# Kernel optimization log

Measured on AMD Instinct MI355X. Metric: run time of the kernel, lower is better.

The kernel has to match this reference:

```python
import jax, jax.numpy as jnp
import numpy as np

B, N, C_IN, C_OUT, K, KS = 8, 2048, 64, 64, 20, 20


def _paiconv(x, feature, kernals, one_padding, mlp_w, mlp_b, conv_w, conv_b,
             mlp_out_w, mlp_out_b, bn_gamma, bn_beta):
    b, c, n = feature.shape
    pts = jnp.transpose(x, (0, 2, 1))                       # [B,N,3]
    sq = jnp.sum(pts * pts, axis=-1)                        # [B,N]
    d2 = sq[:, :, None] + sq[:, None, :] - 2.0 * jnp.einsum('bnd,bmd->bnm', pts, pts)
    _, idx = jax.lax.top_k(-d2, K)                          # [B,N,K] nearest (self first)
    bidx = jnp.arange(b)[:, None, None]
    x_neighs = pts[bidx, idx].reshape(b * n, K, 3)          # [BN,K,3]
    x_repeat = jnp.broadcast_to(x_neighs[:, :1, :], x_neighs.shape)
    x_rel = x_neighs - x_repeat                             # [BN,K,3]
    x_dis = jnp.sqrt(jnp.sum(x_rel * x_rel, axis=-1, keepdims=True) + 1e-12)
    x_feats7 = jnp.concatenate([x_repeat, x_rel, x_dis], axis=-1)  # [BN,K,7]
    # pointwise MLP (Conv1d 7->in_c, kernel 1)
    x_feats = jnp.einsum('nkc,oc->nok', x_feats7, mlp_w) + mlp_b[None, :, None]  # [BN,C,K]
    featsT = jnp.transpose(feature, (0, 2, 1))              # [B,N,C]
    neigh_feats = featsT[bidx, idx].reshape(b * n, K, c)    # [BN,K,C]
    feats = jnp.concatenate([jnp.transpose(neigh_feats, (0, 2, 1)), x_feats], axis=1)  # [BN,2C,K]
    # permutation matrix with threshold + double normalization (topkmax)
    perm = jnp.einsum('nkd,dm->nkm', x_rel, kernals) + one_padding  # [BN,K,KS]
    perm = jnp.where(perm > 0, perm, 0.0)
    perm = perm / (jnp.sum(perm, axis=1, keepdims=True) + 1e-6)
    perm = perm * perm
    perm = perm / (jnp.sum(perm, axis=1, keepdims=True) + 1e-6)
    perm = jnp.where(perm > 0.1, perm, 0.0)
    agg = jnp.einsum('nck,nkm->ncm', feats, perm).reshape(b * n, 2 * c * KS)
    out = (agg @ conv_w.T + conv_b).reshape(b, n, C_OUT)
    out = jnp.transpose(out, (0, 2, 1)) \
        + jnp.einsum('bcn,oc->bon', feature, mlp_out_w) + mlp_out_b[None, :, None]
    # BatchNorm1d (training-mode batch stats, biased variance, eps=1e-5)
    mean = jnp.mean(out, axis=(0, 2), keepdims=True)
    var = jnp.var(out, axis=(0, 2), keepdims=True)
    out = (out - mean) / jnp.sqrt(var + 1e-5)
    return out * bn_gamma[None, :, None] + bn_beta[None, :, None]


def setup_inputs() -> dict:
    key = jax.random.key(0)
    ks = jax.random.split(key, 10)
    one_padding = jnp.zeros((K, KS), jnp.float32).at[0, 0].set(1.0)
    return {
        'x': jax.random.normal(ks[0], (B, 3, N), jnp.float32),
        'feature': jax.random.normal(ks[1], (B, C_IN, N), jnp.float32),
        'kernals': jax.random.normal(ks[2], (3, KS), jnp.float32),
        'one_padding': one_padding,
        'mlp_w': jax.random.normal(ks[3], (C_IN, 7), jnp.float32) * 0.2,
        'mlp_b': jnp.zeros((C_IN,), jnp.float32),
        'conv_w': jax.random.normal(ks[4], (C_OUT, 2 * C_IN * KS), jnp.float32) * 0.02,
        'conv_b': jnp.zeros((C_OUT,), jnp.float32),
        'mlp_out_w': jax.random.normal(ks[5], (C_OUT, C_IN), jnp.float32) * 0.1,
        'mlp_out_b': jnp.zeros((C_OUT,), jnp.float32),
        'bn_gamma': jnp.ones((C_OUT,), jnp.float32),
        'bn_beta': jnp.zeros((C_OUT,), jnp.float32),
    }


def reference(x, feature, kernals, one_padding, mlp_w, mlp_b, conv_w, conv_b,
              mlp_out_w, mlp_out_b, bn_gamma, bn_beta):
    return _paiconv(x, feature, kernals, one_padding, mlp_w, mlp_b, conv_w, conv_b,
                    mlp_out_w, mlp_out_b, bn_gamma, bn_beta)
```

## Files before the change

kernel.cpp:

```cpp
#include <hip/hip_runtime.h>
#include <cstddef>

#define BB   8
#define NN   2048
#define CIN  64
#define COUT 64
#define KK   20
#define KSS  20
#define C2   128
#define PPB  4
#define NC   24
#define KT   80
#define AGG_LD 2576

typedef _Float16 h2t  __attribute__((ext_vector_type(2)));
typedef _Float16 f16x8 __attribute__((ext_vector_type(8)));
typedef float    f32x4 __attribute__((ext_vector_type(4)));

__device__ __forceinline__ unsigned pk2(float a, float b) {
    unsigned short ua = __builtin_bit_cast(unsigned short, (_Float16)a);
    unsigned short ub = __builtin_bit_cast(unsigned short, (_Float16)b);
    return (unsigned)ua | ((unsigned)ub << 16);
}

__device__ __forceinline__ unsigned wave_min_u32(unsigned v) {
    unsigned x = v, t;
    t = (unsigned)__builtin_amdgcn_update_dpp((int)x, (int)x, 0x111, 0xf, 0xf, false);
    x = (t < x) ? t : x;
    t = (unsigned)__builtin_amdgcn_update_dpp((int)x, (int)x, 0x112, 0xf, 0xf, false);
    x = (t < x) ? t : x;
    t = (unsigned)__builtin_amdgcn_update_dpp((int)x, (int)x, 0x114, 0xf, 0xf, false);
    x = (t < x) ? t : x;
    t = (unsigned)__builtin_amdgcn_update_dpp((int)x, (int)x, 0x118, 0xf, 0xf, false);
    x = (t < x) ? t : x;
    t = (unsigned)__builtin_amdgcn_update_dpp((int)x, (int)x, 0x142, 0xf, 0xf, false);
    x = (t < x) ? t : x;
    t = (unsigned)__builtin_amdgcn_update_dpp((int)x, (int)x, 0x143, 0xf, 0xf, false);
    x = (t < x) ? t : x;
    return (unsigned)__builtin_amdgcn_readlane((int)x, 63);
}

__global__ __launch_bounds__(256) void prep_kernel(
    const float* __restrict__ cw, const float* __restrict__ mw,
    uint4* __restrict__ aFrag, float* __restrict__ mowT)
{
    int i = blockIdx.x * 256 + threadIdx.x;
    if (i < 4 * KT * 64) {
        int wv = i / (KT * 64);
        int r  = i - wv * (KT * 64);
        int t  = r >> 6, l = r & 63;
        int o  = (wv << 4) + (l & 15);
        int j  = (t << 5) + ((l >> 4) << 3);
        const float* s = cw + (size_t)o * (C2 * KSS) + j;
        uint4 v;
        v.x = pk2(s[0], s[1]);
        v.y = pk2(s[2], s[3]);
        v.z = pk2(s[4], s[5]);
        v.w = pk2(s[6], s[7]);
        aFrag[i] = v;
    }
    if (i < COUT * CIN) {
        int o = i >> 6, c = i & 63;
        mowT[c * COUT + o] = mw[o * CIN + c];
    }
}

__global__ __launch_bounds__(256) void tr_kernel(
    const float* __restrict__ f, float* __restrict__ ft)
{
    __shared__ float tile[64][65];
    const int bt = blockIdx.x;
    const int b  = bt >> 5;
    const int n0 = (bt & 31) << 6;
    const int tn  = threadIdx.x & 63;
    const int tc0 = threadIdx.x >> 6;
#pragma unroll
    for (int r = 0; r < 16; ++r) {
        int c = (r << 2) + tc0;
        tile[c][tn] = f[((size_t)(b * CIN + c)) * NN + n0 + tn];
    }
    __syncthreads();
#pragma unroll
    for (int r = 0; r < 16; ++r) {
        int n = (r << 2) + tc0;
        ft[((size_t)b * NN + n0 + n) * CIN + tn] = tile[tn][n];
    }
}

__global__ __launch_bounds__(256, 4) void knn_kernel(
    const float* __restrict__ x, int* __restrict__ nid)
{
    const int tid  = threadIdx.x;
    const int w    = tid >> 6;
    const int lane = tid & 63;
    const int p    = blockIdx.x * 4 + w;
    const int b    = p >> 11;
    const int n    = p & (NN - 1);

    const float* xb0 = x + (size_t)(b * 3 + 0) * NN;
    const float* xb1 = x + (size_t)(b * 3 + 1) * NN;
    const float* xb2 = x + (size_t)(b * 3 + 2) * NN;

    const unsigned long long SENT = 0xFFFFFFFFFFFFFFFFull;
    const float qx = xb0[n], qy = xb1[n], qz = xb2[n];

    float d2r[32];
#pragma unroll
    for (int j = 0; j < 32; ++j) {
        int m = lane + 64 * j;
        float dx = xb0[m] - qx;
        float dy = xb1[m] - qy;
        float dz = xb2[m] - qz;
        d2r[j] = dx * dx + dy * dy + dz * dz;
    }

    unsigned long long c0 = SENT, c1 = SENT, c2 = SENT;
#pragma unroll
    for (int j = 0; j < 32; ++j) {
        unsigned long long pk =
            ((unsigned long long)__float_as_uint(d2r[j]) << 32)
            | (unsigned)(lane + 64 * j);
        if (pk < c0)      { c2 = c1; c1 = c0; c0 = pk; }
        else if (pk < c1) { c2 = c1; c1 = pk; }
        else if (pk < c2) { c2 = pk; }
    }

    unsigned killmask = 0u;
    unsigned long long mypk = SENT;
    for (int k = 0; k < NC; ++k) {
        unsigned myd  = (unsigned)(c0 >> 32);
        unsigned dmin = wave_min_u32(myd);
        unsigned idxc = (myd == dmin) ? (unsigned)c0 : 0xFFFFFFFFu;
        unsigned imin = wave_min_u32(idxc);
        unsigned long long bp = ((unsigned long long)dmin << 32) | imin;

        if (lane == k) mypk = bp;
        if (c0 == bp) {
            killmask |= 1u << ((unsigned)(bp & 0xFFFFFFFFull) >> 6);
            c0 = c1; c1 = c2; c2 = SENT;
            if (c0 == SENT) {
#pragma unroll
                for (int j = 0; j < 32; ++j) {
                    if (!(killmask & (1u << j))) {
                        unsigned long long pk =
                            ((unsigned long long)__float_as_uint(d2r[j]) << 32)
                            | (unsigned)(lane + 64 * j);
                        if (pk < c0)      { c2 = c1; c1 = c0; c0 = pk; }
                        else if (pk < c1) { c2 = c1; c1 = pk; }
                        else if (pk < c2) { c2 = pk; }
                    }
                }
            }
        }
    }

    double dd = 1e300;
    int ci = 0x7fffffff;
    if (lane < NC) {
        ci = (int)(mypk & 0xFFFFFFFFull);
        double dx = (double)xb0[ci] - (double)qx;
        double dy = (double)xb1[ci] - (double)qy;
        double dz = (double)xb2[ci] - (double)qz;
        dd = dx * dx + dy * dy + dz * dz;
    }
    unsigned long long db = __double_as_longlong(dd);
#pragma unroll
    for (int size = 2; size <= 32; size <<= 1) {
#pragma unroll
        for (int stride = size >> 1; stride > 0; stride >>= 1) {
            unsigned long long odb = __shfl_xor(db, stride);
            int oci = __shfl_xor(ci, stride);
            bool up = ((lane & size) == 0);
            bool takemin = (((lane & stride) == 0) == up);
            bool oless = (odb < db) || (odb == db && oci < ci);
            if (takemin == oless) { db = odb; ci = oci; }
        }
    }
    if (lane < KK) nid[(size_t)p * KK + lane] = ci;
}

__global__ __launch_bounds__(256, 3) void point_kernel(
    const float* __restrict__ x,
    const float* __restrict__ featT,
    const float* __restrict__ kern,
    const float* __restrict__ pad,
    const float* __restrict__ mlp_w,
    const float* __restrict__ mlp_b,
    const uint4* __restrict__ aFrag,
    const float* __restrict__ conv_b,
    const float* __restrict__ mowT,
    const float* __restrict__ mob,
    const int* __restrict__ nid,
    float* __restrict__ out)
{
    __shared__ __align__(16) _Float16 agg_h[PPB][AGG_LD];
    __shared__ __align__(16) float u_s[PPB * KK * KSS];
    __shared__ float xr_s[PPB][KK][3];
    __shared__ float xd_s[PPB][KK];
    __shared__ float xrep_s[PPB][3];
    __shared__ float colden_s[PPB][KSS];
    __shared__ float fcol_s[PPB][CIN];
    __shared__ int   nid_s[PPB][KK];

    float (*perm_s)[KK][KSS] = (float (*)[KK][KSS])u_s;
    float (*red2)[COUT]      = (float (*)[COUT])u_s;

    const int tid  = threadIdx.x;
    const int w    = tid >> 6;
    const int lane = tid & 63;
    const int p    = blockIdx.x * PPB + w;
    const int b    = p >> 11;
    const int n    = p & (NN - 1);

    const float* xb0 = x + (size_t)(b * 3 + 0) * NN;
    const float* xb1 = x + (size_t)(b * 3 + 1) * NN;
    const float* xb2 = x + (size_t)(b * 3 + 2) * NN;

    if (lane < KK) nid_s[w][lane] = nid[(size_t)p * KK + lane];

    fcol_s[w][lane] = featT[((size_t)b * NN + n) * CIN + lane];

    if (lane == 0) {
        int m0 = nid_s[w][0];
        xrep_s[w][0] = xb0[m0]; xrep_s[w][1] = xb1[m0]; xrep_s[w][2] = xb2[m0];
    }
    if (lane < KK) {
        int m = nid_s[w][lane];
        float rx = xb0[m] - xrep_s[w][0];
        float ry = xb1[m] - xrep_s[w][1];
        float rz = xb2[m] - xrep_s[w][2];
        xr_s[w][lane][0] = rx; xr_s[w][lane][1] = ry; xr_s[w][lane][2] = rz;
        xd_s[w][lane] = sqrtf(rx * rx + ry * ry + rz * rz + 1e-12f);
    }

    for (int e = lane; e < KK * KSS; e += 64) {
        int k = e / KSS, m = e % KSS;
        float v = xr_s[w][k][0] * kern[0 * KSS + m]
                + xr_s[w][k][1] * kern[1 * KSS + m]
                + xr_s[w][k][2] * kern[2 * KSS + m]
                + pad[k * KSS + m];
        perm_s[w][k][m] = v > 0.0f ? v : 0.0f;
    }
    if (lane < KSS) {
        float s = 0.0f;
        for (int k = 0; k < KK; ++k) s += perm_s[w][k][lane];
        colden_s[w][lane] = s + 1e-6f;
    }
    for (int e = lane; e < KK * KSS; e += 64) {
        int k = e / KSS, m = e % KSS;
        float v = perm_s[w][k][m] / colden_s[w][m];
        perm_s[w][k][m] = v * v;
    }
    if (lane < KSS) {
        float s = 0.0f;
        for (int k = 0; k < KK; ++k) s += perm_s[w][k][lane];
        colden_s[w][lane] = s + 1e-6f;
    }
    for (int e = lane; e < KK * KSS; e += 64) {
        int k = e / KSS, m = e % KSS;
        float v = perm_s[w][k][m] / colden_s[w][m];
        perm_s[w][k][m] = v > 0.1f ? v : 0.0f;
    }

    float fg[KK], fm[KK];
#pragma unroll
    for (int k = 0; k < KK; ++k)
        fg[k] = featT[((size_t)b * NN + nid_s[w][k]) * CIN + lane];
    {
        float w0 = mlp_w[lane * 7 + 0], w1 = mlp_w[lane * 7 + 1];
        float w2 = mlp_w[lane * 7 + 2], w3 = mlp_w[lane * 7 + 3];
        float w4 = mlp_w[lane * 7 + 4], w5 = mlp_w[lane * 7 + 5];
        float w6 = mlp_w[lane * 7 + 6];
        float bias = mlp_b[lane];
#pragma unroll
        for (int k = 0; k < KK; ++k) {
            fm[k] = xrep_s[w][0] * w0 + xrep_s[w][1] * w1 + xrep_s[w][2] * w2
                  + xr_s[w][k][0] * w3 + xr_s[w][k][1] * w4 + xr_s[w][k][2] * w5
                  + xd_s[w][k] * w6 + bias;
        }
    }

#pragma unroll
    for (int m4 = 0; m4 < KSS / 4; ++m4) {
        float sx = 0.f, sy = 0.f, sz = 0.f, sw = 0.f;
        float tx = 0.f, ty = 0.f, tz = 0.f, tw = 0.f;
#pragma unroll
        for (int k = 0; k < KK; ++k) {
            const float4 pv = *(const float4*)&perm_s[w][k][m4 * 4];
            const float a = fg[k], c = fm[k];
            sx += a * pv.x; sy += a * pv.y; sz += a * pv.z; sw += a * pv.w;
            tx += c * pv.x; ty += c * pv.y; tz += c * pv.z; tw += c * pv.w;
        }
        const int mb = m4 * 4;
        agg_h[w][lane * KSS + mb + 0]         = (_Float16)sx;
        agg_h[w][lane * KSS + mb + 1]         = (_Float16)sy;
        agg_h[w][lane * KSS + mb + 2]         = (_Float16)sz;
        agg_h[w][lane * KSS + mb + 3]         = (_Float16)sw;
        agg_h[w][(CIN + lane) * KSS + mb + 0] = (_Float16)tx;
        agg_h[w][(CIN + lane) * KSS + mb + 1] = (_Float16)ty;
        agg_h[w][(CIN + lane) * KSS + mb + 2] = (_Float16)tz;
        agg_h[w][(CIN + lane) * KSS + mb + 3] = (_Float16)tw;
    }
    __syncthreads();

    {
        f32x4 acc0 = {0.f, 0.f, 0.f, 0.f};
        f32x4 acc1 = {0.f, 0.f, 0.f, 0.f};
        const uint4* ap = aFrag + (size_t)(w * KT) * 64 + lane;
        const _Float16* bp = &agg_h[lane & 3][(lane >> 4) * 8];
#pragma unroll 4
        for (int t = 0; t < KT; t += 2) {
            uint4 av0 = ap[(size_t)t * 64];
            uint4 av1 = ap[(size_t)(t + 1) * 64];
            f16x8 b0 = *(const f16x8*)(bp + t * 32);
            f16x8 b1 = *(const f16x8*)(bp + (t + 1) * 32);
            acc0 = __builtin_amdgcn_mfma_f32_16x16x32_f16(
                       __builtin_bit_cast(f16x8, av0), b0, acc0, 0, 0, 0);
            acc1 = __builtin_amdgcn_mfma_f32_16x16x32_f16(
                       __builtin_bit_cast(f16x8, av1), b1, acc1, 0, 0, 0);
        }
        acc0 += acc1;
        if ((lane & 15) < 4) {
            const int p2 = lane & 15;
            const int ob = (w << 4) + ((lane >> 4) << 2);
            *(f32x4*)&red2[p2][ob] = acc0;
        }
    }
    __syncthreads();

    {
        float acc = conv_b[lane] + red2[w][lane];
        for (int c = 0; c < CIN; ++c)
            acc += fcol_s[w][c] * mowT[c * COUT + lane];
        acc += mob[lane];
        out[(size_t)(b * COUT + lane) * NN + n] = acc;
    }
}

__global__ __launch_bounds__(256) void bn_reduce(
    const float* __restrict__ out, float* __restrict__ part)
{
    const int o = blockIdx.x >> 3;
    const int s = blockIdx.x & 7;
    const float* src = out + (size_t)(s * COUT + o) * NN;
    float a = 0.f, q = 0.f;
    for (int i = threadIdx.x; i < NN; i += 256) {
        float v = src[i];
        a += v; q += v * v;
    }
    __shared__ float s1[256], s2[256];
    s1[threadIdx.x] = a; s2[threadIdx.x] = q;
    __syncthreads();
    for (int st = 128; st > 0; st >>= 1) {
        if (threadIdx.x < st) {
            s1[threadIdx.x] += s1[threadIdx.x + st];
            s2[threadIdx.x] += s2[threadIdx.x + st];
        }
        __syncthreads();
    }
    if (threadIdx.x == 0) {
        part[(o * 8 + s) * 2 + 0] = s1[0];
        part[(o * 8 + s) * 2 + 1] = s2[0];
    }
}

__global__ __launch_bounds__(256) void bn_apply(
    float* __restrict__ out, const float* __restrict__ part,
    const float* __restrict__ gamma, const float* __restrict__ beta)
{
    const int o = blockIdx.x >> 3;
    const int s = blockIdx.x & 7;
    float a = 0.f, q = 0.f;
#pragma unroll
    for (int t = 0; t < 8; ++t) {
        a += part[(o * 8 + t) * 2 + 0];
        q += part[(o * 8 + t) * 2 + 1];
    }
    const float M = (float)(BB * NN);
    const float mean = a / M;
    float var = q / M - mean * mean;
    if (var < 0.f) var = 0.f;
    const float inv = 1.0f / sqrtf(var + 1e-5f);
    const float g = gamma[o] * inv, be = beta[o];
    float* dst = out + (size_t)(s * COUT + o) * NN;
    for (int i = threadIdx.x; i < NN; i += 256) {
        dst[i] = (dst[i] - mean) * g + be;
    }
}

extern "C" void kernel_launch(void* const* d_in, const int* in_sizes, int n_in,
                              void* d_out, int out_size, void* d_ws, size_t ws_size,
                              hipStream_t stream)
{
    const float* x       = (const float*)d_in[0];
    const float* feature = (const float*)d_in[1];
    const float* kern    = (const float*)d_in[2];
    const float* pad     = (const float*)d_in[3];
    const float* mlp_w   = (const float*)d_in[4];
    const float* mlp_b   = (const float*)d_in[5];
    const float* conv_w  = (const float*)d_in[6];
    const float* conv_b  = (const float*)d_in[7];
    const float* mow     = (const float*)d_in[8];
    const float* mob     = (const float*)d_in[9];
    const float* gamma   = (const float*)d_in[10];
    const float* beta    = (const float*)d_in[11];

    char* wsp = (char*)d_ws;
    uint4* aFrag = (uint4*)wsp;
    float* mowT  = (float*)(wsp + 327680);
    float* part  = (float*)(wsp + 327680 + 16384);
    int*   nid   = (int*)(wsp + 327680 + 16384 + 4096);
    float* featT = (float*)(wsp + 327680 + 16384 + 4096 + 1310720);

    float* out = (float*)d_out;

    prep_kernel<<<(4 * KT * 64 + 255) / 256, 256, 0, stream>>>(conv_w, mow, aFrag, mowT);
    tr_kernel<<<BB * (NN / 64), 256, 0, stream>>>(feature, featT);
    knn_kernel<<<BB * NN / 4, 256, 0, stream>>>(x, nid);
    point_kernel<<<BB * NN / PPB, 256, 0, stream>>>(x, featT, kern, pad,
                                                    mlp_w, mlp_b, aFrag, conv_b,
                                                    mowT, mob, nid, out);
    bn_reduce<<<512, 256, 0, stream>>>(out, part);
    bn_apply<<<512, 256, 0, stream>>>(out, part, gamma, beta);
}
```

Baseline: 249.8 us.

## Replace iterative KNN selection with radix threshold search and ballot compaction

The kNN kernel now loads coordinates with float4 vector loads and keeps a per-lane top-4 list. It finds the 24th-smallest distance with a 31-step bitwise radix search driven by ballots, then compacts the candidates through shared memory. This replaces 24 rounds of double wave-min reductions. The old iterative path stays as a fallback when the threshold is ambiguous or a lane's top-4 list is exhausted. Separately, point_kernel's launch bounds are raised to 4 waves per SIMD, which may force register spills.

```diff
diff --git a/kernel.cpp b/kernel.cpp
--- a/kernel.cpp
+++ b/kernel.cpp
@@ -38,6 +38,12 @@
     t = (unsigned)__builtin_amdgcn_update_dpp((int)x, (int)x, 0x143, 0xf, 0xf, false);
     x = (t < x) ? t : x;
     return (unsigned)__builtin_amdgcn_readlane((int)x, 63);
+}
+
+__device__ __forceinline__ float d2f(float px, float py, float pz,
+                                     float qx, float qy, float qz) {
+    float dx = px - qx, dy = py - qy, dz = pz - qz;
+    return fmaf(dz, dz, fmaf(dy, dy, dx * dx));
 }
 
 __global__ __launch_bounds__(256) void prep_kernel(
@@ -90,6 +96,8 @@
 __global__ __launch_bounds__(256, 4) void knn_kernel(
     const float* __restrict__ x, int* __restrict__ nid)
 {
+    __shared__ int cand_s[4][32];
+
     const int tid  = threadIdx.x;
     const int w    = tid >> 6;
     const int lane = tid & 63;
@@ -105,59 +113,97 @@
     const float qx = xb0[n], qy = xb1[n], qz = xb2[n];
 
     float d2r[32];
-#pragma unroll
-    for (int j = 0; j < 32; ++j) {
-        int m = lane + 64 * j;
-        float dx = xb0[m] - qx;
-        float dy = xb1[m] - qy;
-        float dz = xb2[m] - qz;
-        d2r[j] = dx * dx + dy * dy + dz * dz;
-    }
-
-    unsigned long long c0 = SENT, c1 = SENT, c2 = SENT;
-#pragma unroll
-    for (int j = 0; j < 32; ++j) {
-        unsigned long long pk =
-            ((unsigned long long)__float_as_uint(d2r[j]) << 32)
-            | (unsigned)(lane + 64 * j);
-        if (pk < c0)      { c2 = c1; c1 = c0; c0 = pk; }
-        else if (pk < c1) { c2 = c1; c1 = pk; }
-        else if (pk < c2) { c2 = pk; }
-    }
-
-    unsigned killmask = 0u;
-    unsigned long long mypk = SENT;
-    for (int k = 0; k < NC; ++k) {
-        unsigned myd  = (unsigned)(c0 >> 32);
-        unsigned dmin = wave_min_u32(myd);
-        unsigned idxc = (myd == dmin) ? (unsigned)c0 : 0xFFFFFFFFu;
-        unsigned imin = wave_min_u32(idxc);
-        unsigned long long bp = ((unsigned long long)dmin << 32) | imin;
-
-        if (lane == k) mypk = bp;
-        if (c0 == bp) {
-            killmask |= 1u << ((unsigned)(bp & 0xFFFFFFFFull) >> 6);
-            c0 = c1; c1 = c2; c2 = SENT;
-            if (c0 == SENT) {
-#pragma unroll
-                for (int j = 0; j < 32; ++j) {
-                    if (!(killmask & (1u << j))) {
+    unsigned long long c0 = SENT, c1 = SENT, c2 = SENT, c3 = SENT;
+#pragma unroll
+    for (int jj = 0; jj < 8; ++jj) {
+        const int m0 = jj * 256 + lane * 4;
+        const float4 vx = *(const float4*)&xb0[m0];
+        const float4 vy = *(const float4*)&xb1[m0];
+        const float4 vz = *(const float4*)&xb2[m0];
+        const float dd4[4] = { d2f(vx.x, vy.x, vz.x, qx, qy, qz),
+                               d2f(vx.y, vy.y, vz.y, qx, qy, qz),
+                               d2f(vx.z, vy.z, vz.z, qx, qy, qz),
+                               d2f(vx.w, vy.w, vz.w, qx, qy, qz) };
+#pragma unroll
+        for (int e = 0; e < 4; ++e) {
+            d2r[(jj << 2) | e] = dd4[e];
+            unsigned long long pk =
+                ((unsigned long long)__float_as_uint(dd4[e]) << 32)
+                | (unsigned)(m0 + e);
+            if (pk < c0)      { c3 = c2; c2 = c1; c1 = c0; c0 = pk; }
+            else if (pk < c1) { c3 = c2; c2 = c1; c1 = pk; }
+            else if (pk < c2) { c3 = c2; c2 = pk; }
+            else if (pk < c3) { c3 = pk; }
+        }
+    }
+
+    const unsigned dv0 = (unsigned)(c0 >> 32), dv1 = (unsigned)(c1 >> 32);
+    const unsigned dv2 = (unsigned)(c2 >> 32), dv3 = (unsigned)(c3 >> 32);
+
+    unsigned pfx = 0u;
+    for (int i = 30; i >= 0; --i) {
+        unsigned T = pfx | (1u << i);
+        int cnt = (int)(dv0 < T) + (int)(dv1 < T) + (int)(dv2 < T) + (int)(dv3 < T);
+        unsigned long long B0 = __ballot(cnt & 1);
+        unsigned long long B1 = __ballot(cnt & 2);
+        unsigned long long B2 = __ballot(cnt & 4);
+        int tot = __popcll(B0) + 2 * __popcll(B1) + 4 * __popcll(B2);
+        if (tot < NC) pfx = T;
+    }
+    const unsigned tau = pfx;
+
+    int cle = (int)(dv0 <= tau) + (int)(dv1 <= tau)
+            + (int)(dv2 <= tau) + (int)(dv3 <= tau);
+    unsigned long long L0 = __ballot(cle & 1);
+    unsigned long long L1 = __ballot(cle & 2);
+    unsigned long long L2 = __ballot(cle & 4);
+    int tot_le = __popcll(L0) + 2 * __popcll(L1) + 4 * __popcll(L2);
+    const bool trigger = (tot_le != NC) || (__ballot(cle == 4) != 0ull);
+
+    int ci_cand = 0x7fffffff;
+    if (!trigger) {
+        unsigned long long below = (1ull << lane) - 1ull;
+        int pre = __popcll(L0 & below) + 2 * __popcll(L1 & below);
+        if (cle >= 1) cand_s[w][pre + 0] = (int)(unsigned)c0;
+        if (cle >= 2) cand_s[w][pre + 1] = (int)(unsigned)c1;
+        if (cle >= 3) cand_s[w][pre + 2] = (int)(unsigned)c2;
+        if (lane < NC) ci_cand = cand_s[w][lane];
+    } else {
+        unsigned killmask = 0u;
+        unsigned long long mypk = SENT;
+        for (int k = 0; k < NC; ++k) {
+            unsigned myd  = (unsigned)(c0 >> 32);
+            unsigned dmin = wave_min_u32(myd);
+            unsigned idxc = (myd == dmin) ? (unsigned)c0 : 0xFFFFFFFFu;
+            unsigned imin = wave_min_u32(idxc);
+            unsigned long long bp = ((unsigned long long)dmin << 32) | imin;
+            if (lane == k) mypk = bp;
+            if (c0 == bp) {
+                unsigned mi = (unsigned)(bp & 0xFFFFFFFFull);
+                killmask |= 1u << (((mi >> 8) << 2) | (mi & 3));
+                c0 = c1; c1 = c2; c2 = c3; c3 = SENT;
+                if (c0 == SENT) {
+                    for (int s = 0; s < 32; ++s) {
+                        if (killmask & (1u << s)) continue;
+                        int m = ((s >> 2) << 8) + lane * 4 + (s & 3);
                         unsigned long long pk =
-                            ((unsigned long long)__float_as_uint(d2r[j]) << 32)
-                            | (unsigned)(lane + 64 * j);
-                        if (pk < c0)      { c2 = c1; c1 = c0; c0 = pk; }
-                        else if (pk < c1) { c2 = c1; c1 = pk; }
-                        else if (pk < c2) { c2 = pk; }
+                            ((unsigned long long)__float_as_uint(d2r[s]) << 32)
+                            | (unsigned)m;
+                        if (pk < c0)      { c3 = c2; c2 = c1; c1 = c0; c0 = pk; }
+                        else if (pk < c1) { c3 = c2; c2 = c1; c1 = pk; }
+                        else if (pk < c2) { c3 = c2; c2 = pk; }
+                        else if (pk < c3) { c3 = pk; }
                     }
                 }
             }
         }
+        if (lane < NC) ci_cand = (int)(mypk & 0xFFFFFFFFull);
     }
 
     double dd = 1e300;
     int ci = 0x7fffffff;
     if (lane < NC) {
-        ci = (int)(mypk & 0xFFFFFFFFull);
+        ci = ci_cand;
         double dx = (double)xb0[ci] - (double)qx;
         double dy = (double)xb1[ci] - (double)qy;
         double dz = (double)xb2[ci] - (double)qz;
@@ -179,7 +225,7 @@
     if (lane < KK) nid[(size_t)p * KK + lane] = ci;
 }
 
-__global__ __launch_bounds__(256, 3) void point_kernel(
+__global__ __launch_bounds__(256, 4) void point_kernel(
     const float* __restrict__ x,
     const float* __restrict__ featT,
     const float* __restrict__ kern,
```

Result: slower. 311.5 us (+24.7%).
